# Kernel optimization log

Hardware: AMD Instinct MI355X
Metric: run time of the kernel (lower is better)

The kernel has to match this reference:

```python
import jax, jax.numpy as jnp
import numpy as np

N_USER = 100000
N_ITEM = 50000
N = N_USER + N_ITEM          # total graph nodes
D = 64                        # embed_size
NNZ = 4_000_000               # nonzeros in normalized adjacency
LAYERS = 3
B = 2048                      # batch_size
NEG = 4 * B                   # 4 negatives per positive (see create_bpr_loss)


def setup_inputs() -> dict:
    key = jax.random.key(0)
    ks = jax.random.split(key, 8)
    user_emb = jax.random.normal(ks[0], (N_USER, D), dtype=jnp.float32) * 0.1
    item_emb = jax.random.normal(ks[1], (N_ITEM, D), dtype=jnp.float32) * 0.1
    adj_row = jax.random.randint(ks[2], (NNZ,), 0, N, dtype=jnp.int32)
    adj_col = jax.random.randint(ks[3], (NNZ,), 0, N, dtype=jnp.int32)
    # symmetric-normalized adjacency values are small positive floats
    adj_val = jax.random.uniform(ks[4], (NNZ,), dtype=jnp.float32) * 0.05
    users = jax.random.randint(ks[5], (B,), 0, N_USER, dtype=jnp.int32)
    pos_items = jax.random.randint(ks[6], (B,), 0, N_ITEM, dtype=jnp.int32)
    neg_items = jax.random.randint(ks[7], (NEG,), 0, N_ITEM, dtype=jnp.int32)
    mask = jnp.zeros((1,), dtype=jnp.float32)      # unused in mode='plain'
    norm_adj = jnp.zeros((1,), dtype=jnp.float32)  # unused when attention=False
    return {
        "users": users, "pos_items": pos_items, "neg_items": neg_items,
        "mask": mask, "norm_adj": norm_adj,
        "user_emb": user_emb, "item_emb": item_emb,
        "adj_row": adj_row, "adj_col": adj_col, "adj_val": adj_val,
    }


def _spmm(row, col, val, x):
    """Sparse [N,N] @ dense [N,D] via gather + segment_sum."""
    gathered = val[:, None] * x[col]                      # [NNZ, D]
    return jax.ops.segment_sum(gathered, row, num_segments=N)


def reference(users, pos_items, neg_items, mask, norm_adj,
              user_emb, item_emb, adj_row, adj_col, adj_val):
    # ego embeddings for all nodes
    e0 = jnp.concatenate([user_emb, item_emb], axis=0)    # [N, D]
    # NOTE: the original torch code never updates ego_embeddings inside the
    # layer loop, so every layer appends the SAME A_hat @ E0. Hence:
    # light_out = mean([E0, A@E0, A@E0, ..., A@E0]) = (E0 + L*A@E0)/(L+1)
    ae0 = _spmm(adj_row, adj_col, adj_val, e0)            # [N, D]
    light_out = (e0 + LAYERS * ae0) / (LAYERS + 1)
    u_g = light_out[:N_USER]
    i_g = light_out[N_USER:]
    u_g_embeddings = u_g[users]
    pos_i_g_embeddings = i_g[pos_items]
    neg_i_g_embeddings = i_g[neg_items]
    return (u_g_embeddings, pos_i_g_embeddings, neg_i_g_embeddings)
```

## Files before the change

kernel.cpp:

```cpp
#include <hip/hip_runtime.h>

#define N_USER 100000
#define N_ITEM 50000
#define NTOT   150000
#define D      64
#define NNZ    4000000
#define B      2048
#define NEG    8192
#define NSLOT  (B + B + NEG)
#define CAP    128

__device__ __forceinline__ int slot_row(int slot,
                                        const int* __restrict__ users,
                                        const int* __restrict__ pos,
                                        const int* __restrict__ neg) {
    if (slot < B)     return users[slot];
    if (slot < 2 * B) return N_USER + pos[slot - B];
    return N_USER + neg[slot - 2 * B];
}

__device__ __forceinline__ const float* e0_row(int c,
                                               const float* __restrict__ ue,
                                               const float* __restrict__ ie) {
    return (c < N_USER) ? &ue[(size_t)c * D] : &ie[(size_t)(c - N_USER) * D];
}

__global__ void k_clear(int* __restrict__ slotmap) {
    int i = blockIdx.x * blockDim.x + threadIdx.x;
    if (i < NTOT) slotmap[i] = -1;
}

__global__ void k_mark(const int* __restrict__ users,
                       const int* __restrict__ pos,
                       const int* __restrict__ neg,
                       int* __restrict__ slotmap,
                       int* __restrict__ cnt,
                       float* __restrict__ accd) {
    int slot = (blockIdx.x * blockDim.x + threadIdx.x) >> 6;
    int lane = threadIdx.x & 63;
    if (slot >= NSLOT) return;
    int r = slot_row(slot, users, pos, neg);
    int old = 0;
    if (lane == 0) old = atomicCAS(&slotmap[r], -1, slot);
    old = __shfl(old, 0);
    if (old == -1) {
        if (lane == 0) cnt[slot] = 0;
        accd[(size_t)slot * D + lane] = 0.0f;
    }
}

__global__ void k_scan(const int*   __restrict__ adj_row,
                       const int*   __restrict__ adj_col,
                       const float* __restrict__ adj_val,
                       const float* __restrict__ ue,
                       const float* __restrict__ ie,
                       const int*   __restrict__ slotmap,
                       int*   __restrict__ cnt,
                       int*   __restrict__ bcol,
                       float* __restrict__ bval,
                       float* __restrict__ accd) {
    int tid = blockIdx.x * blockDim.x + threadIdx.x;
    int nth = gridDim.x * blockDim.x;
    for (int e = tid; e < NNZ; e += nth) {
        int r = adj_row[e];
        int s = slotmap[r];
        if (s >= 0) {
            int   c = adj_col[e];
            float v = adj_val[e];
            int idx = atomicAdd(&cnt[s], 1);
            if (idx < CAP) {
                bcol[s * CAP + idx] = c;
                bval[s * CAP + idx] = v;
            } else {
                const float* x = e0_row(c, ue, ie);
                for (int d = 0; d < D; ++d)
                    atomicAdd(&accd[(size_t)s * D + d], v * x[d]);
            }
        }
    }
}

__global__ void k_rowacc(const int* __restrict__ users,
                         const int* __restrict__ pos,
                         const int* __restrict__ neg,
                         const int* __restrict__ slotmap,
                         const int* __restrict__ cnt,
                         const int* __restrict__ bcol,
                         const float* __restrict__ bval,
                         const float* __restrict__ ue,
                         const float* __restrict__ ie,
                         float* __restrict__ accd) {
    int slot = (blockIdx.x * blockDim.x + threadIdx.x) >> 6;
    int lane = threadIdx.x & 63;
    if (slot >= NSLOT) return;
    int r = slot_row(slot, users, pos, neg);
    if (slotmap[r] != slot) return;
    int n = cnt[slot];
    if (n > CAP) n = CAP;
    const int*   bc = &bcol[slot * CAP];
    const float* bv = &bval[slot * CAP];
    float a = 0.0f;
    int i = 0;
    for (; i + 4 <= n; i += 4) {
        int c0 = bc[i], c1 = bc[i + 1], c2 = bc[i + 2], c3 = bc[i + 3];
        float v0 = bv[i], v1 = bv[i + 1], v2 = bv[i + 2], v3 = bv[i + 3];
        float x0 = e0_row(c0, ue, ie)[lane];
        float x1 = e0_row(c1, ue, ie)[lane];
        float x2 = e0_row(c2, ue, ie)[lane];
        float x3 = e0_row(c3, ue, ie)[lane];
        a += v0 * x0;
        a += v1 * x1;
        a += v2 * x2;
        a += v3 * x3;
    }
    for (; i < n; ++i) a += bv[i] * e0_row(bc[i], ue, ie)[lane];
    accd[(size_t)slot * D + lane] += a;
}

__global__ void k_out(const int* __restrict__ users,
                      const int* __restrict__ pos,
                      const int* __restrict__ neg,
                      const float* __restrict__ ue,
                      const float* __restrict__ ie,
                      const int* __restrict__ slotmap,
                      const float* __restrict__ accd,
                      float* __restrict__ out) {
    int slot = (blockIdx.x * blockDim.x + threadIdx.x) >> 6;
    int lane = threadIdx.x & 63;
    if (slot >= NSLOT) return;
    int r = slot_row(slot, users, pos, neg);
    float e = (r < N_USER) ? ue[(size_t)r * D + lane]
                           : ie[(size_t)(r - N_USER) * D + lane];
    int id = slotmap[r];
    out[(size_t)slot * D + lane] = 0.25f * e + 0.75f * accd[(size_t)id * D + lane];
}

extern "C" void kernel_launch(void* const* d_in, const int* in_sizes, int n_in,
                              void* d_out, int out_size, void* d_ws, size_t ws_size,
                              hipStream_t stream) {
    const int*   users   = (const int*)  d_in[0];
    const int*   pos     = (const int*)  d_in[1];
    const int*   neg     = (const int*)  d_in[2];
    const float* ue      = (const float*)d_in[5];
    const float* ie      = (const float*)d_in[6];
    const int*   adj_row = (const int*)  d_in[7];
    const int*   adj_col = (const int*)  d_in[8];
    const float* adj_val = (const float*)d_in[9];
    float*       out     = (float*)      d_out;

    char* w = (char*)d_ws;
    int*   slotmap = (int*)w;   w += (size_t)NTOT * sizeof(int);
    int*   cnt     = (int*)w;   w += (size_t)NSLOT * sizeof(int);
    int*   bcol    = (int*)w;   w += (size_t)NSLOT * CAP * sizeof(int);
    float* bval    = (float*)w; w += (size_t)NSLOT * CAP * sizeof(float);
    float* accd    = (float*)w;

    k_clear <<<(NTOT + 255) / 256, 256, 0, stream>>>(slotmap);
    k_mark  <<<(NSLOT * 64 + 255) / 256, 256, 0, stream>>>(users, pos, neg,
                                                           slotmap, cnt, accd);
    k_scan  <<<2048, 256, 0, stream>>>(adj_row, adj_col, adj_val, ue, ie,
                                       slotmap, cnt, bcol, bval, accd);
    k_rowacc<<<(NSLOT * 64 + 255) / 256, 256, 0, stream>>>(users, pos, neg,
                                                           slotmap, cnt, bcol, bval,
                                                           ue, ie, accd);
    k_out   <<<(NSLOT * 64 + 255) / 256, 256, 0, stream>>>(users, pos, neg, ue, ie,
                                                           slotmap, accd, out);
}
```

Measured before the change: 194.7 us.

## Filter edges with shared-memory row bitmap, vectorize scan, pack col/val pairs

Adds a bitmap of selected rows that each scan block copies into LDS (about 18.7KB), so testing an edge's row no longer needs a random global slotmap read. The edge arrays are read as int4/float4 to cut load instructions. Column and value are packed into one int2 bucket entry, and the row accumulation loop is unrolled by 8 for more loads in flight. The cost is a per-block bitmap copy across 2048 blocks and more LDS use per block, which may lower occupancy.

```diff
diff --git a/kernel.cpp b/kernel.cpp
--- a/kernel.cpp
+++ b/kernel.cpp
@@ -9,6 +9,7 @@
 #define NEG    8192
 #define NSLOT  (B + B + NEG)
 #define CAP    128
+#define NBW    ((NTOT + 31) / 32)
 
 __device__ __forceinline__ int slot_row(int slot,
                                         const int* __restrict__ users,
@@ -25,15 +26,17 @@
     return (c < N_USER) ? &ue[(size_t)c * D] : &ie[(size_t)(c - N_USER) * D];
 }
 
-__global__ void k_clear(int* __restrict__ slotmap) {
+__global__ void k_clear(int* __restrict__ slotmap, unsigned int* __restrict__ bits) {
     int i = blockIdx.x * blockDim.x + threadIdx.x;
     if (i < NTOT) slotmap[i] = -1;
+    if (i < NBW)  bits[i] = 0u;
 }
 
 __global__ void k_mark(const int* __restrict__ users,
                        const int* __restrict__ pos,
                        const int* __restrict__ neg,
                        int* __restrict__ slotmap,
+                       unsigned int* __restrict__ bits,
                        int* __restrict__ cnt,
                        float* __restrict__ accd) {
     int slot = (blockIdx.x * blockDim.x + threadIdx.x) >> 6;
@@ -44,7 +47,10 @@
     if (lane == 0) old = atomicCAS(&slotmap[r], -1, slot);
     old = __shfl(old, 0);
     if (old == -1) {
-        if (lane == 0) cnt[slot] = 0;
+        if (lane == 0) {
+            cnt[slot] = 0;
+            atomicOr(&bits[r >> 5], 1u << (r & 31));
+        }
         accd[(size_t)slot * D + lane] = 0.0f;
     }
 }
@@ -54,29 +60,49 @@
                        const float* __restrict__ adj_val,
                        const float* __restrict__ ue,
                        const float* __restrict__ ie,
+                       const unsigned int* __restrict__ bits,
                        const int*   __restrict__ slotmap,
                        int*   __restrict__ cnt,
-                       int*   __restrict__ bcol,
-                       float* __restrict__ bval,
+                       int2*  __restrict__ bcv,
                        float* __restrict__ accd) {
+    __shared__ unsigned int sbits[NBW];
+    {
+        const int4* gb = (const int4*)bits;
+        int4* sb = (int4*)sbits;
+        for (int i = threadIdx.x; i < NBW / 4; i += blockDim.x) sb[i] = gb[i];
+    }
+    __syncthreads();
+
     int tid = blockIdx.x * blockDim.x + threadIdx.x;
     int nth = gridDim.x * blockDim.x;
-    for (int e = tid; e < NNZ; e += nth) {
-        int r = adj_row[e];
-        int s = slotmap[r];
-        if (s >= 0) {
-            int   c = adj_col[e];
-            float v = adj_val[e];
-            int idx = atomicAdd(&cnt[s], 1);
-            if (idx < CAP) {
-                bcol[s * CAP + idx] = c;
-                bval[s * CAP + idx] = v;
-            } else {
-                const float* x = e0_row(c, ue, ie);
-                for (int d = 0; d < D; ++d)
-                    atomicAdd(&accd[(size_t)s * D + d], v * x[d]);
-            }
+    const int4*   row4 = (const int4*)adj_row;
+    const int4*   col4 = (const int4*)adj_col;
+    const float4* val4 = (const float4*)adj_val;
+
+    for (int g = tid; g < NNZ / 4; g += nth) {
+        int4   r = row4[g];
+        int4   c = col4[g];
+        float4 v = val4[g];
+        #define PROC(RR, CC, VV)                                               \
+        {                                                                      \
+            unsigned int w = sbits[(RR) >> 5];                                 \
+            if ((w >> ((RR) & 31)) & 1u) {                                     \
+                int s = slotmap[RR];                                           \
+                int idx = atomicAdd(&cnt[s], 1);                               \
+                if (idx < CAP) {                                               \
+                    bcv[s * CAP + idx] = make_int2(CC, __float_as_int(VV));    \
+                } else {       \
+                    const float* x = e0_row(CC, ue, ie);                       \
+                    for (int d = 0; d < D; ++d)                                \
+                        atomicAdd(&accd[(size_t)s * D + d], (VV) * x[d]);      \
+                }                                                              \
+            }                                                                  \
         }
+        PROC(r.x, c.x, v.x)
+        PROC(r.y, c.y, v.y)
+        PROC(r.z, c.z, v.z)
+        PROC(r.w, c.w, v.w)
+        #undef PROC
     }
 }
 
@@ -85,8 +111,7 @@
                          const int* __restrict__ neg,
                          const int* __restrict__ slotmap,
                          const int* __restrict__ cnt,
-                         const int* __restrict__ bcol,
-                         const float* __restrict__ bval,
+                         const int2* __restrict__ bcv,
                          const float* __restrict__ ue,
                          const float* __restrict__ ie,
                          float* __restrict__ accd) {
@@ -97,23 +122,33 @@
     if (slotmap[r] != slot) return;
     int n = cnt[slot];
     if (n > CAP) n = CAP;
-    const int*   bc = &bcol[slot * CAP];
-    const float* bv = &bval[slot * CAP];
+    const int2* bb = &bcv[slot * CAP];
     float a = 0.0f;
     int i = 0;
-    for (; i + 4 <= n; i += 4) {
-        int c0 = bc[i], c1 = bc[i + 1], c2 = bc[i + 2], c3 = bc[i + 3];
-        float v0 = bv[i], v1 = bv[i + 1], v2 = bv[i + 2], v3 = bv[i + 3];
-        float x0 = e0_row(c0, ue, ie)[lane];
-        float x1 = e0_row(c1, ue, ie)[lane];
-        float x2 = e0_row(c2, ue, ie)[lane];
-        float x3 = e0_row(c3, ue, ie)[lane];
-        a += v0 * x0;
-        a += v1 * x1;
-        a += v2 * x2;
-        a += v3 * x3;
-    }
-    for (; i < n; ++i) a += bv[i] * e0_row(bc[i], ue, ie)[lane];
+    for (; i + 8 <= n; i += 8) {
+        int2 p0 = bb[i],     p1 = bb[i + 1], p2 = bb[i + 2], p3 = bb[i + 3];
+        int2 p4 = bb[i + 4], p5 = bb[i + 5], p6 = bb[i + 6], p7 = bb[i + 7];
+        float x0 = e0_row(p0.x, ue, ie)[lane];
+        float x1 = e0_row(p1.x, ue, ie)[lane];
+        float x2 = e0_row(p2.x, ue, ie)[lane];
+        float x3 = e0_row(p3.x, ue, ie)[lane];
+        float x4 = e0_row(p4.x, ue, ie)[lane];
+        float x5 = e0_row(p5.x, ue, ie)[lane];
+        float x6 = e0_row(p6.x, ue, ie)[lane];
+        float x7 = e0_row(p7.x, ue, ie)[lane];
+        a += __int_as_float(p0.y) * x0;
+        a += __int_as_float(p1.y) * x1;
+        a += __int_as_float(p2.y) * x2;
+        a += __int_as_float(p3.y) * x3;
+        a += __int_as_float(p4.y) * x4;
+        a += __int_as_float(p5.y) * x5;
+        a += __int_as_float(p6.y) * x6;
+        a += __int_as_float(p7.y) * x7;
+    }
+    for (; i < n; ++i) {
+        int2 p = bb[i];
+        a += __int_as_float(p.y) * e0_row(p.x, ue, ie)[lane];
+    }
     accd[(size_t)slot * D + lane] += a;
 }
 
@@ -149,19 +184,19 @@
     float*       out     = (float*)      d_out;
 
     char* w = (char*)d_ws;
-    int*   slotmap = (int*)w;   w += (size_t)NTOT * sizeof(int);
-    int*   cnt     = (int*)w;   w += (size_t)NSLOT * sizeof(int);
-    int*   bcol    = (int*)w;   w += (size_t)NSLOT * CAP * sizeof(int);
-    float* bval    = (float*)w; w += (size_t)NSLOT * CAP * sizeof(float);
-    float* accd    = (float*)w;
-
-    k_clear <<<(NTOT + 255) / 256, 256, 0, stream>>>(slotmap);
+    int*          slotmap = (int*)w;          w += (size_t)NTOT * sizeof(int);
+    unsigned int* bits    = (unsigned int*)w; w += (size_t)NBW * sizeof(unsigned int);
+    int*          cnt     = (int*)w;          w += (size_t)NSLOT * sizeof(int);
+    int2*         bcv     = (int2*)w;         w += (size_t)NSLOT * CAP * sizeof(int2);
+    float*        accd    = (float*)w;
+
+    k_clear <<<(NTOT + 255) / 256, 256, 0, stream>>>(slotmap, bits);
     k_mark  <<<(NSLOT * 64 + 255) / 256, 256, 0, stream>>>(users, pos, neg,
-                                                           slotmap, cnt, accd);
+                                                           slotmap, bits, cnt, accd);
     k_scan  <<<2048, 256, 0, stream>>>(adj_row, adj_col, adj_val, ue, ie,
-                                       slotmap, cnt, bcol, bval, accd);
+                                       bits, slotmap, cnt, bcv, accd);
     k_rowacc<<<(NSLOT * 64 + 255) / 256, 256, 0, stream>>>(users, pos, neg,
-                                                           slotmap, cnt, bcol, bval,
+                                                           slotmap, cnt, bcv,
                                                            ue, ie, accd);
     k_out   <<<(NSLOT * 64 + 255) / 256, 256, 0, stream>>>(users, pos, neg, ue, ie,
                                                            slotmap, accd, out);
```

After: 170.9 us. 1.14x faster.
